# Performance work log

Hardware: AMD Instinct MI355X
Metric: run time of the kernel (lower is better)

The kernel has to match this reference:

```python
import jax, jax.numpy as jnp
import numpy as np


def log_mat_mul(m1, m2):
    """Log-semiring matmul: AND(a,b) = -logaddexp(-a,-b); OR-reduce = logsumexp over K.
    m1: (B, I, K), m2: (B, K, J) -> (B, I, J)."""
    # (B, I, 1, K) vs (B, 1, J, K)
    z = -jnp.logaddexp(-m1[:, :, None, :], -jnp.swapaxes(m2, -1, -2)[:, None, :, :])
    return jax.nn.logsumexp(z, axis=-1)


def cum_mul(m):
    """Parallel-doubling inclusive cumulative log-semiring product over axis 1.
    m: (B, L, D, D) -> (B, L, D, D) with m_out[:, j] = m[:,0] * ... * m[:,j]."""
    B, L, D, _ = m.shape
    step = 1
    while step < L:
        m4 = log_mat_mul(m[:, : L - step].reshape(-1, D, D),
                         m[:, step:].reshape(-1, D, D))
        m = jnp.concatenate([m[:, :step], m4.reshape(B, -1, D, D)], axis=1)
        step *= 2
    return m


def setup_inputs() -> dict:
    key = jax.random.key(0)
    k1, k2 = jax.random.split(key)
    B, L, D, A = 8, 64, 64, 4
    act = jax.random.randint(k1, (B, L), 0, A)  # action ids in [0, n_act)
    p = jax.random.normal(k2, (A + 1, D, D), dtype=jnp.float32)  # transition params
    init_vec = jnp.full((D,), 5.0, dtype=jnp.float32)            # nn.Parameter init
    return {"p": p, "init_vec": init_vec, "act": act}


def reference(p, init_vec, act):
    B, L = act.shape
    D = init_vec.shape[0]
    # state(act): gather per-step transition matrices (noise = 0.0)
    pm = p[act + 1]                      # (B, L, D, D)
    pm = cum_mul(pm)                     # cumulative products along L
    x = log_mat_mul(jnp.broadcast_to(init_vec.reshape(1, 1, D), (B * L, 1, D)),
                    pm.reshape(-1, D, D))  # (B*L, 1, D)
    x = x.reshape(B, L, D)
    # obs(state): one more log-semiring matmul against p[0]
    # y[b,l,j] = logsumexp_k( -logaddexp(-x[b,l,k], -p0[k,j]) )
    y = jax.nn.logsumexp(-jnp.logaddexp(-x[..., :, None], -p[0]), axis=-2)
    return y
```

## Files before the change

### kernel.cpp

```cpp
#include <hip/hip_runtime.h>
#include <hip/hip_bf16.h>


#define MAT 4096
#define NMAT 512
#define ARS 68
#define TBL_MATS 20

typedef float f32x2 __attribute__((ext_vector_type(2)));

__device__ __forceinline__ float rcpf(float x) { return __builtin_amdgcn_rcpf(x); }

__device__ __forceinline__ bool probe_f32(const void* initv) {
    return (*(const unsigned int*)initv) == 0x40A00000u;
}
__device__ __forceinline__ float load_in(const void* p, int i, bool isf32) {
    return isf32 ? ((const float*)p)[i]
                 : __bfloat162float(((const __hip_bfloat16*)p)[i]);
}

__device__ __forceinline__ const float* mat_src(int b, int x, int rnow,
                                                const float* bufA, const float* bufB,
                                                const float* tbl, const int* act) {
    const int la = (x == 0) ? 1 : (32 - __clz(x));
    const int lr = (la > rnow - 1) ? (rnow - 1) : la;
    if (lr == 1) {
        const float* T = tbl + b * TBL_MATS * MAT;
        if (x == 0) return T + act[b * 64] * MAT;
        return T + (4 + act[b * 64 + x - 1] * 4 + act[b * 64 + x]) * MAT;
    }
    const float* buf = (lr & 1) ? bufB : bufA;
    return buf + (b * 64 + x) * MAT;
}

__device__ __forceinline__ f32x2 quad2(const float a[4], f32x2 b0, f32x2 b1,
                                       f32x2 b2, f32x2 b3) {
#pragma clang fp contract(fast)
    const f32x2 x0 = b0 + a[0], x1 = b1 + a[1], x2 = b2 + a[2], x3 = b3 + a[3];
    const f32x2 n1 = x0 + x1, d1 = x0 * x1;
    const f32x2 n2 = x2 + x3, d2 = x2 * x3;
    const f32x2 num = n1 * d2 + n2 * d1;
    const f32x2 den = d1 * d2;
    f32x2 r;
    r.x = rcpf(den.x);
    r.y = rcpf(den.y);
    return num * r;
}

__device__ __forceinline__ void inner_round(const float* As, const float* Bs,
                                            int t, float4 out[2]) {
    const int r = t >> 4, c0 = (t & 15) * 4;
    f32x2 acc[2][2] = {{{0.f,0.f},{0.f,0.f}},{{0.f,0.f},{0.f,0.f}}};
    #pragma unroll
    for (int kq = 0; kq < 16; ++kq) {
        float a0[4], a1[4];
        f32x2 b[4][2];
        { const float4 v = *(const float4*)(As + r * ARS + kq * 4);
          a0[0]=v.x; a0[1]=v.y; a0[2]=v.z; a0[3]=v.w; }
        { const float4 v = *(const float4*)(As + (r + 16) * ARS + kq * 4);
          a1[0]=v.x; a1[1]=v.y; a1[2]=v.z; a1[3]=v.w; }
        #pragma unroll
        for (int kk = 0; kk < 4; ++kk) {
            const float4 v = *(const float4*)(Bs + (kq * 4 + kk) * 64 + c0);
            b[kk][0] = f32x2{v.x, v.y};
            b[kk][1] = f32x2{v.z, v.w};
        }
        #pragma unroll
        for (int cp = 0; cp < 2; ++cp) {
            acc[0][cp] += quad2(a0, b[0][cp], b[1][cp], b[2][cp], b[3][cp]);
            acc[1][cp] += quad2(a1, b[0][cp], b[1][cp], b[2][cp], b[3][cp]);
        }
    }
    out[0] = make_float4(rcpf(acc[0][0].x), rcpf(acc[0][0].y),
                         rcpf(acc[0][1].x), rcpf(acc[0][1].y));
    out[1] = make_float4(rcpf(acc[1][0].x), rcpf(acc[1][0].y),
                         rcpf(acc[1][1].x), rcpf(acc[1][1].y));
}

__device__ __forceinline__ void inner_full(const float* As, const float* Bs,
                                           int t, float4 out[4]) {
    const int r = t >> 4, c0 = (t & 15) * 4;
    f32x2 acc[4][2];
    #pragma unroll
    for (int i = 0; i < 4; ++i) { acc[i][0] = f32x2{0.f,0.f}; acc[i][1] = f32x2{0.f,0.f}; }
    #pragma unroll
    for (int kq = 0; kq < 16; ++kq) {
        float av[4][4];
        f32x2 b[4][2];
        #pragma unroll
        for (int i = 0; i < 4; ++i) {
            const float4 v = *(const float4*)(As + (r + i * 16) * ARS + kq * 4);
            av[i][0]=v.x; av[i][1]=v.y; av[i][2]=v.z; av[i][3]=v.w;
        }
        #pragma unroll
        for (int kk = 0; kk < 4; ++kk) {
            const float4 v = *(const float4*)(Bs + (kq * 4 + kk) * 64 + c0);
            b[kk][0] = f32x2{v.x, v.y};
            b[kk][1] = f32x2{v.z, v.w};
        }
        #pragma unroll
        for (int i = 0; i < 4; ++i)
            #pragma unroll
            for (int cp = 0; cp < 2; ++cp)
                acc[i][cp] += quad2(av[i], b[0][cp], b[1][cp], b[2][cp], b[3][cp]);
    }
    #pragma unroll
    for (int i = 0; i < 4; ++i)
        out[i] = make_float4(rcpf(acc[i][0].x), rcpf(acc[i][0].y),
                             rcpf(acc[i][1].x), rcpf(acc[i][1].y));
}

__device__ __forceinline__ void stage_A(float* As, const float* src, int t) {
    const float4* sa = (const float4*)src;
    #pragma unroll
    for (int i = 0; i < 2; ++i) {
        const int fi = t + i * 256;
        const float4 v = sa[fi];
        *(float4*)(As + (fi >> 4) * ARS + (fi & 15) * 4) = v;
    }
}
__device__ __forceinline__ void stage_B(float* Bs, const float* src, int t) {
    const float4* sb = (const float4*)src;
    #pragma unroll
    for (int i = 0; i < 4; ++i) ((float4*)Bs)[t + i * 256] = sb[t + i * 256];
}

__global__ __launch_bounds__(256, 4)
void k_table(const void* __restrict__ pIn, float* __restrict__ tbl,
             const void* __restrict__ initIn) {
    const bool isf32 = probe_f32(initIn);
    const int b = blockIdx.x & 7, job = blockIdx.x >> 3, t = threadIdx.x;
    float* T = tbl + b * TBL_MATS * MAT;

    if (job < 8) {
        const int a = job >> 1, rs = (job & 1) << 5;
        const int base = (a + 1) * MAT + rs * 64;
        float* d = T + a * MAT + rs * 64;
        #pragma unroll
        for (int i = 0; i < 8; ++i) {
            const int idx = t + i * 256;
            d[idx] = __expf(-load_in(pIn, base + idx, isf32));
        }
        return;
    }
    const int pj = job - 8, pairIdx = pj >> 1, rs = (pj & 1) << 5;
    const int a1 = pairIdx >> 2, a2 = pairIdx & 3;
    __shared__ float As[32 * ARS];
    __shared__ float Bs[MAT];
    const int baseA = (a1 + 1) * MAT + rs * 64;
    const int baseB = (a2 + 1) * MAT;
    #pragma unroll
    for (int i = 0; i < 8; ++i) {
        const int idx = t + i * 256;
        As[(idx >> 6) * ARS + (idx & 63)] = __expf(-load_in(pIn, baseA + idx, isf32));
    }
    #pragma unroll
    for (int i = 0; i < 16; ++i) {
        const int idx = t + i * 256;
        Bs[idx] = __expf(-load_in(pIn, baseB + idx, isf32));
    }
    __syncthreads();
    float4 o[2];
    inner_round(As, Bs, t, o);
    float* d = T + (4 + pairIdx) * MAT;
    const int r = t >> 4, c0 = (t & 15) * 4;
    *(float4*)(d + (rs + r) * 64 + c0) = o[0];
    *(float4*)(d + (rs + r + 16) * 64 + c0) = o[1];
}

__global__ __launch_bounds__(256, 4)
void k_round(const float* __restrict__ bufA, const float* __restrict__ bufB,
             const float* __restrict__ tbl, const int* __restrict__ act,
             float* __restrict__ dst, int step, int rnow) {
    const int t = threadIdx.x;
    const int b = blockIdx.x & 7, job = blockIdx.x >> 3;
    const int rs = (job & 1) << 5, mIdx = job >> 1;
    const int j = step + mIdx;
    const int m = b * 64 + j, ja = j - step;

    __shared__ float As[32 * ARS];
    __shared__ float Bs[MAT];
    stage_A(As, mat_src(b, ja, rnow, bufA, bufB, tbl, act) + rs * 64, t);
    stage_B(Bs, mat_src(b, j, rnow, bufA, bufB, tbl, act), t);
    __syncthreads();
    float4 o[2];
    inner_round(As, Bs, t, o);
    const int rr = t >> 4, c0 = (t & 15) * 4;
    *(float4*)(dst + m * MAT + (rs + rr) * 64 + c0) = o[0];
    *(float4*)(dst + m * MAT + (rs + rr + 16) * 64 + c0) = o[1];
}

__global__ __launch_bounds__(256, 2)
void k_final6(const float* __restrict__ bufA, const float* __restrict__ bufB,
              const float* __restrict__ tbl, const int* __restrict__ act,
              const void* __restrict__ pIn, const void* __restrict__ initIn,
              void* __restrict__ out) {
    const bool isf32 = probe_f32(initIn);
    const int t = threadIdx.x;
    const int b = blockIdx.x & 7, j = blockIdx.x >> 3;
    const int m = b * 64 + j;
    __shared__ float As[64 * ARS];
    __shared__ float Bs[MAT];
    __shared__ float red[4 * 64];
    __shared__ float uxs[64];
    __shared__ float uin[64];
    if (t < 64) uin[t] = __expf(-load_in(initIn, t, isf32));

    if (j >= 32) {
        const int ja = j - 32;
        const float* Asrc = mat_src(b, ja, 6, bufA, bufB, tbl, act);
        {
            const float4* sa = (const float4*)Asrc;
            #pragma unroll
            for (int i = 0; i < 4; ++i) {
                const int fi = t + i * 256;
                const float4 v = sa[fi];
                *(float4*)(As + (fi >> 4) * ARS + (fi & 15) * 4) = v;
            }
        }
        stage_B(Bs, mat_src(b, j, 6, bufA, bufB, tbl, act), t);
        __syncthreads();
        float4 o[4];
        inner_full(As, Bs, t, o);
        __syncthreads();
        const int r = t >> 4, c0 = (t & 15) * 4;
        #pragma unroll
        for (int i = 0; i < 4; ++i)
            *(float4*)(Bs + (r + i * 16) * 64 + c0) = o[i];
    } else {
        stage_B(Bs, mat_src(b, j, 7, bufA, bufB, tbl, act), t);
    }
    __syncthreads();

    const int jj = t & 63, kq = t >> 6;
    float s = 0.f;
    #pragma unroll
    for (int kk = 0; kk < 16; ++kk) {
        const int k = kq * 16 + kk;
        s += rcpf(uin[k] + Bs[k * 64 + jj]);
    }
    red[kq * 64 + jj] = s;
    __syncthreads();
    if (t < 64)
        uxs[t] = rcpf(((red[t] + red[64 + t]) + red[128 + t]) + red[192 + t]);
    __syncthreads();

    float s2 = 0.f;
    #pragma unroll
    for (int kk = 0; kk < 16; ++kk) {
        const int k = kq * 16 + kk;
        s2 += rcpf(uxs[k] + __expf(-load_in(pIn, k * 64 + jj, isf32)));
    }
    red[kq * 64 + jj] = s2;
    __syncthreads();
    if (t < 64) {
        const float y = __logf(((red[t] + red[64 + t]) + red[128 + t]) + red[192 + t]);
        if (isf32) ((float*)out)[m * 64 + t] = y;
        else       ((__hip_bfloat16*)out)[m * 64 + t] = __float2bfloat16(y);
    }
}

extern "C" void kernel_launch(void* const* d_in, const int* in_sizes, int n_in,
                              void* d_out, int out_size, void* d_ws, size_t ws_size,
                              hipStream_t stream) {
    const void* p = d_in[0];
    const void* initv = d_in[1];
    const int* act = (const int*)d_in[2];

    float* bufA = (float*)d_ws;
    float* bufB = bufA + NMAT * MAT;
    float* tbl  = bufB + NMAT * MAT;

    k_table<<<40 * 8, 256, 0, stream>>>(p, tbl, initv);
    k_round<<<62 * 2 * 8, 256, 0, stream>>>(bufA, bufB, tbl, act, bufA, 2, 2);
    k_round<<<60 * 2 * 8, 256, 0, stream>>>(bufA, bufB, tbl, act, bufB, 4, 3);
    k_round<<<56 * 2 * 8, 256, 0, stream>>>(bufA, bufB, tbl, act, bufA, 8, 4);
    k_round<<<48 * 2 * 8, 256, 0, stream>>>(bufA, bufB, tbl, act, bufB, 16, 5);
    k_final6<<<64 * 8, 256, 0, stream>>>(bufA, bufB, tbl, act, p, initv, d_out);
}
```

Baseline: 61.92 us.

## Fuse doubling scan rounds into three kernels with redundant in-block recomputation

Replaces the table kernel, four round kernels and final kernel with three 512-thread kernels. Each block recomputes up to two levels of the doubling scan locally in shared memory, so the three launches together cover the prefix products. This removes launch count and the global round-trips between rounds. In exchange, each block does up to three 64x64 semiring matmuls and needs more shared memory per block, which may lower occupancy.

```diff
diff --git a/kernel.cpp b/kernel.cpp
--- a/kernel.cpp
+++ b/kernel.cpp
@@ -5,7 +5,6 @@
 #define MAT 4096
 #define NMAT 512
 #define ARS 68
-#define TBL_MATS 20
 
 typedef float f32x2 __attribute__((ext_vector_type(2)));
 
@@ -17,20 +16,6 @@
 __device__ __forceinline__ float load_in(const void* p, int i, bool isf32) {
     return isf32 ? ((const float*)p)[i]
                  : __bfloat162float(((const __hip_bfloat16*)p)[i]);
-}
-
-__device__ __forceinline__ const float* mat_src(int b, int x, int rnow,
-                                                const float* bufA, const float* bufB,
-                                                const float* tbl, const int* act) {
-    const int la = (x == 0) ? 1 : (32 - __clz(x));
-    const int lr = (la > rnow - 1) ? (rnow - 1) : la;
-    if (lr == 1) {
-        const float* T = tbl + b * TBL_MATS * MAT;
-        if (x == 0) return T + act[b * 64] * MAT;
-        return T + (4 + act[b * 64 + x - 1] * 4 + act[b * 64 + x]) * MAT;
-    }
-    const float* buf = (lr & 1) ? bufB : bufA;
-    return buf + (b * 64 + x) * MAT;
 }
 
 __device__ __forceinline__ f32x2 quad2(const float a[4], f32x2 b0, f32x2 b1,
@@ -47,8 +32,8 @@
     return num * r;
 }
 
-__device__ __forceinline__ void inner_round(const float* As, const float* Bs,
-                                            int t, float4 out[2]) {
+__device__ __forceinline__ void inner512(const float* As, const float* Bs,
+                                         int t, float4 out[2]) {
     const int r = t >> 4, c0 = (t & 15) * 4;
     f32x2 acc[2][2] = {{{0.f,0.f},{0.f,0.f}},{{0.f,0.f},{0.f,0.f}}};
     #pragma unroll
@@ -57,7 +42,7 @@
         f32x2 b[4][2];
         { const float4 v = *(const float4*)(As + r * ARS + kq * 4);
           a0[0]=v.x; a0[1]=v.y; a0[2]=v.z; a0[3]=v.w; }
-        { const float4 v = *(const float4*)(As + (r + 16) * ARS + kq * 4);
+        { const float4 v = *(const float4*)(As + (r + 32) * ARS + kq * 4);
           a1[0]=v.x; a1[1]=v.y; a1[2]=v.z; a1[3]=v.w; }
         #pragma unroll
         for (int kk = 0; kk < 4; ++kk) {
@@ -77,184 +62,238 @@
                          rcpf(acc[1][1].x), rcpf(acc[1][1].y));
 }
 
-__device__ __forceinline__ void inner_full(const float* As, const float* Bs,
-                                           int t, float4 out[4]) {
+__device__ __forceinline__ void write2(float* dst, int stride, int t, const float4 o[2]) {
     const int r = t >> 4, c0 = (t & 15) * 4;
-    f32x2 acc[4][2];
-    #pragma unroll
-    for (int i = 0; i < 4; ++i) { acc[i][0] = f32x2{0.f,0.f}; acc[i][1] = f32x2{0.f,0.f}; }
-    #pragma unroll
-    for (int kq = 0; kq < 16; ++kq) {
-        float av[4][4];
-        f32x2 b[4][2];
-        #pragma unroll
-        for (int i = 0; i < 4; ++i) {
-            const float4 v = *(const float4*)(As + (r + i * 16) * ARS + kq * 4);
-            av[i][0]=v.x; av[i][1]=v.y; av[i][2]=v.z; av[i][3]=v.w;
-        }
-        #pragma unroll
-        for (int kk = 0; kk < 4; ++kk) {
-            const float4 v = *(const float4*)(Bs + (kq * 4 + kk) * 64 + c0);
-            b[kk][0] = f32x2{v.x, v.y};
-            b[kk][1] = f32x2{v.z, v.w};
-        }
-        #pragma unroll
-        for (int i = 0; i < 4; ++i)
-            #pragma unroll
-            for (int cp = 0; cp < 2; ++cp)
-                acc[i][cp] += quad2(av[i], b[0][cp], b[1][cp], b[2][cp], b[3][cp]);
-    }
-    #pragma unroll
-    for (int i = 0; i < 4; ++i)
-        out[i] = make_float4(rcpf(acc[i][0].x), rcpf(acc[i][0].y),
-                             rcpf(acc[i][1].x), rcpf(acc[i][1].y));
-}
-
-__device__ __forceinline__ void stage_A(float* As, const float* src, int t) {
-    const float4* sa = (const float4*)src;
+    *(float4*)(dst + r * stride + c0) = o[0];
+    *(float4*)(dst + (r + 32) * stride + c0) = o[1];
+}
+
+__device__ __forceinline__ void stage_pad(float* D, const float* src, int t) {
+    const float4* s = (const float4*)src;
     #pragma unroll
     for (int i = 0; i < 2; ++i) {
-        const int fi = t + i * 256;
-        const float4 v = sa[fi];
-        *(float4*)(As + (fi >> 4) * ARS + (fi & 15) * 4) = v;
-    }
-}
-__device__ __forceinline__ void stage_B(float* Bs, const float* src, int t) {
-    const float4* sb = (const float4*)src;
-    #pragma unroll
-    for (int i = 0; i < 4; ++i) ((float4*)Bs)[t + i * 256] = sb[t + i * 256];
-}
-
-__global__ __launch_bounds__(256, 4)
-void k_table(const void* __restrict__ pIn, float* __restrict__ tbl,
-             const void* __restrict__ initIn) {
+        const int fi = t + i * 512;
+        const float4 v = s[fi];
+        *(float4*)(D + (fi >> 4) * ARS + (fi & 15) * 4) = v;
+    }
+}
+__device__ __forceinline__ void stage_row(float* D, const float* src, int t) {
+    const float4* s = (const float4*)src;
+    ((float4*)D)[t] = s[t];
+    ((float4*)D)[t + 512] = s[t + 512];
+}
+__device__ __forceinline__ void stage_pad_exp(float* D, const void* p, int base,
+                                              bool isf32, int t) {
+    #pragma unroll
+    for (int i = 0; i < 8; ++i) {
+        const int idx = t + i * 512;
+        D[(idx >> 6) * ARS + (idx & 63)] = __expf(-load_in(p, base + idx, isf32));
+    }
+}
+__device__ __forceinline__ void stage_row_exp(float* D, const void* p, int base,
+                                              bool isf32, int t) {
+    #pragma unroll
+    for (int i = 0; i < 8; ++i) {
+        const int idx = t + i * 512;
+        D[idx] = __expf(-load_in(p, base + idx, isf32));
+    }
+}
+
+__global__ __launch_bounds__(512, 4)
+void k1(const void* __restrict__ pIn, const int* __restrict__ act,
+        float* __restrict__ bufA, float* __restrict__ bufB,
+        const void* __restrict__ initIn) {
     const bool isf32 = probe_f32(initIn);
-    const int b = blockIdx.x & 7, job = blockIdx.x >> 3, t = threadIdx.x;
-    float* T = tbl + b * TBL_MATS * MAT;
-
-    if (job < 8) {
-        const int a = job >> 1, rs = (job & 1) << 5;
-        const int base = (a + 1) * MAT + rs * 64;
-        float* d = T + a * MAT + rs * 64;
+    const int t = threadIdx.x, b = blockIdx.x & 7, j = blockIdx.x >> 3;
+    const int m = b * 64 + j;
+    const int* a = act + b * 64;
+    __shared__ float As[64 * ARS];
+    __shared__ float Ds[64 * ARS];
+    __shared__ float Bs[MAT];
+    __shared__ float Es[MAT];
+
+    if (j == 0) {
+        const int base = (a[0] + 1) * MAT;
+        float* d = bufB + m * MAT;
         #pragma unroll
         for (int i = 0; i < 8; ++i) {
-            const int idx = t + i * 256;
+            const int idx = t + i * 512;
             d[idx] = __expf(-load_in(pIn, base + idx, isf32));
         }
         return;
     }
-    const int pj = job - 8, pairIdx = pj >> 1, rs = (pj & 1) << 5;
-    const int a1 = pairIdx >> 2, a2 = pairIdx & 3;
-    __shared__ float As[32 * ARS];
-    __shared__ float Bs[MAT];
-    const int baseA = (a1 + 1) * MAT + rs * 64;
-    const int baseB = (a2 + 1) * MAT;
-    #pragma unroll
-    for (int i = 0; i < 8; ++i) {
-        const int idx = t + i * 256;
-        As[(idx >> 6) * ARS + (idx & 63)] = __expf(-load_in(pIn, baseA + idx, isf32));
-    }
-    #pragma unroll
-    for (int i = 0; i < 16; ++i) {
-        const int idx = t + i * 256;
-        Bs[idx] = __expf(-load_in(pIn, baseB + idx, isf32));
+    if (j == 1) {
+        stage_pad_exp(As, pIn, (a[0] + 1) * MAT, isf32, t);
+        stage_row_exp(Bs, pIn, (a[1] + 1) * MAT, isf32, t);
+        __syncthreads();
+        float4 o[2];
+        inner512(As, Bs, t, o);
+        write2(bufB + m * MAT, 64, t, o);
+        return;
+    }
+    if (j == 2) {
+        stage_pad_exp(Ds, pIn, (a[0] + 1) * MAT, isf32, t);
+    } else {
+        stage_pad_exp(As, pIn, (a[j - 3] + 1) * MAT, isf32, t);
+        stage_row_exp(Bs, pIn, (a[j - 2] + 1) * MAT, isf32, t);
+        __syncthreads();
+        float4 o[2];
+        inner512(As, Bs, t, o);
+        write2(Ds, ARS, t, o);
+    }
+    __syncthreads();
+    stage_pad_exp(As, pIn, (a[j - 1] + 1) * MAT, isf32, t);
+    stage_row_exp(Bs, pIn, (a[j] + 1) * MAT, isf32, t);
+    __syncthreads();
+    {
+        float4 o[2];
+        inner512(As, Bs, t, o);
+        write2(Es, 64, t, o);
     }
     __syncthreads();
     float4 o[2];
-    inner_round(As, Bs, t, o);
-    float* d = T + (4 + pairIdx) * MAT;
-    const int r = t >> 4, c0 = (t & 15) * 4;
-    *(float4*)(d + (rs + r) * 64 + c0) = o[0];
-    *(float4*)(d + (rs + r + 16) * 64 + c0) = o[1];
-}
-
-__global__ __launch_bounds__(256, 4)
-void k_round(const float* __restrict__ bufA, const float* __restrict__ bufB,
-             const float* __restrict__ tbl, const int* __restrict__ act,
-             float* __restrict__ dst, int step, int rnow) {
-    const int t = threadIdx.x;
-    const int b = blockIdx.x & 7, job = blockIdx.x >> 3;
-    const int rs = (job & 1) << 5, mIdx = job >> 1;
-    const int j = step + mIdx;
-    const int m = b * 64 + j, ja = j - step;
-
-    __shared__ float As[32 * ARS];
-    __shared__ float Bs[MAT];
-    stage_A(As, mat_src(b, ja, rnow, bufA, bufB, tbl, act) + rs * 64, t);
-    stage_B(Bs, mat_src(b, j, rnow, bufA, bufB, tbl, act), t);
-    __syncthreads();
-    float4 o[2];
-    inner_round(As, Bs, t, o);
-    const int rr = t >> 4, c0 = (t & 15) * 4;
-    *(float4*)(dst + m * MAT + (rs + rr) * 64 + c0) = o[0];
-    *(float4*)(dst + m * MAT + (rs + rr + 16) * 64 + c0) = o[1];
-}
-
-__global__ __launch_bounds__(256, 2)
-void k_final6(const float* __restrict__ bufA, const float* __restrict__ bufB,
-              const float* __restrict__ tbl, const int* __restrict__ act,
-              const void* __restrict__ pIn, const void* __restrict__ initIn,
-              void* __restrict__ out) {
-    const bool isf32 = probe_f32(initIn);
-    const int t = threadIdx.x;
-    const int b = blockIdx.x & 7, j = blockIdx.x >> 3;
+    inner512(Ds, Es, t, o);
+    write2(bufA + m * MAT, 64, t, o);
+}
+
+__global__ __launch_bounds__(512, 4)
+void k2(const float* __restrict__ bufA, float* __restrict__ bufB) {
+    const int t = threadIdx.x, b = blockIdx.x & 7, j = (blockIdx.x >> 3) + 4;
     const int m = b * 64 + j;
     __shared__ float As[64 * ARS];
+    __shared__ float Ds[64 * ARS];
     __shared__ float Bs[MAT];
-    __shared__ float red[4 * 64];
+    __shared__ float Es[MAT];
+
+    #define R2P(y) (((y) < 2 ? bufB : bufA) + (b * 64 + (y)) * MAT)
+
+    if (j < 8) {
+        stage_pad(As, R2P(j - 4), t);
+        stage_row(Bs, R2P(j), t);
+        __syncthreads();
+        float4 o[2];
+        inner512(As, Bs, t, o);
+        write2(bufB + m * MAT, 64, t, o);
+        return;
+    }
+    const int ja = j - 8;
+    if (ja < 4) {
+        stage_pad(Ds, R2P(ja), t);
+    } else {
+        stage_pad(As, R2P(ja - 4), t);
+        stage_row(Bs, R2P(ja), t);
+        __syncthreads();
+        float4 o[2];
+        inner512(As, Bs, t, o);
+        write2(Ds, ARS, t, o);
+    }
+    __syncthreads();
+    stage_pad(As, R2P(j - 4), t);
+    stage_row(Bs, R2P(j), t);
+    __syncthreads();
+    {
+        float4 o[2];
+        inner512(As, Bs, t, o);
+        write2(Es, 64, t, o);
+    }
+    __syncthreads();
+    float4 o[2];
+    inner512(Ds, Es, t, o);
+    write2(bufB + m * MAT, 64, t, o);
+    #undef R2P
+}
+
+__global__ __launch_bounds__(512, 4)
+void k3(const float* __restrict__ bufA, const float* __restrict__ bufB,
+        const void* __restrict__ pIn, const void* __restrict__ initIn,
+        void* __restrict__ out) {
+    const bool isf32 = probe_f32(initIn);
+    const int t = threadIdx.x, b = blockIdx.x & 7, j = blockIdx.x >> 3;
+    const int m = b * 64 + j;
+    __shared__ float As[64 * ARS];
+    __shared__ float Ds[64 * ARS];
+    __shared__ float Bs[MAT];
+    __shared__ float Es[MAT];
+    __shared__ float red[8 * 64];
     __shared__ float uxs[64];
     __shared__ float uin[64];
     if (t < 64) uin[t] = __expf(-load_in(initIn, t, isf32));
 
-    if (j >= 32) {
+    #define ST4(x) ((((x) == 2) || ((x) == 3) ? bufA : bufB) + (b * 64 + (x)) * MAT)
+
+    const float* Up;
+    if (j < 16) {
+        stage_row(Es, ST4(j), t);
+        Up = Es;
+        __syncthreads();
+    } else if (j < 32) {
+        stage_pad(As, ST4(j - 16), t);
+        stage_row(Bs, ST4(j), t);
+        __syncthreads();
+        float4 o[2];
+        inner512(As, Bs, t, o);
+        write2(Es, 64, t, o);
+        Up = Es;
+        __syncthreads();
+    } else {
         const int ja = j - 32;
-        const float* Asrc = mat_src(b, ja, 6, bufA, bufB, tbl, act);
+        if (ja < 16) {
+            stage_pad(Ds, ST4(ja), t);
+        } else {
+            stage_pad(As, ST4(ja - 16), t);
+            stage_row(Bs, ST4(ja), t);
+            __syncthreads();
+            float4 o[2];
+            inner512(As, Bs, t, o);
+            write2(Ds, ARS, t, o);
+            __syncthreads();
+        }
+        stage_pad(As, ST4(j - 16), t);
+        stage_row(Bs, ST4(j), t);
+        __syncthreads();
         {
-            const float4* sa = (const float4*)Asrc;
-            #pragma unroll
-            for (int i = 0; i < 4; ++i) {
-                const int fi = t + i * 256;
-                const float4 v = sa[fi];
-                *(float4*)(As + (fi >> 4) * ARS + (fi & 15) * 4) = v;
-            }
-        }
-        stage_B(Bs, mat_src(b, j, 6, bufA, bufB, tbl, act), t);
-        __syncthreads();
-        float4 o[4];
-        inner_full(As, Bs, t, o);
-        __syncthreads();
-        const int r = t >> 4, c0 = (t & 15) * 4;
-        #pragma unroll
-        for (int i = 0; i < 4; ++i)
-            *(float4*)(Bs + (r + i * 16) * 64 + c0) = o[i];
-    } else {
-        stage_B(Bs, mat_src(b, j, 7, bufA, bufB, tbl, act), t);
-    }
-    __syncthreads();
+            float4 o[2];
+            inner512(As, Bs, t, o);
+            write2(Es, 64, t, o);
+        }
+        __syncthreads();
+        float4 o[2];
+        inner512(Ds, Es, t, o);
+        write2(As, 64, t, o);
+        Up = As;
+        __syncthreads();
+    }
+    #undef ST4
 
     const int jj = t & 63, kq = t >> 6;
     float s = 0.f;
     #pragma unroll
-    for (int kk = 0; kk < 16; ++kk) {
-        const int k = kq * 16 + kk;
-        s += rcpf(uin[k] + Bs[k * 64 + jj]);
+    for (int kk = 0; kk < 8; ++kk) {
+        const int k = kq * 8 + kk;
+        s += rcpf(uin[k] + Up[k * 64 + jj]);
     }
     red[kq * 64 + jj] = s;
     __syncthreads();
-    if (t < 64)
-        uxs[t] = rcpf(((red[t] + red[64 + t]) + red[128 + t]) + red[192 + t]);
-    __syncthreads();
-
+    if (t < 64) {
+        float acc = red[t];
+        #pragma unroll
+        for (int q = 1; q < 8; ++q) acc += red[q * 64 + t];
+        uxs[t] = rcpf(acc);
+    }
+    __syncthreads();
     float s2 = 0.f;
     #pragma unroll
-    for (int kk = 0; kk < 16; ++kk) {
-        const int k = kq * 16 + kk;
+    for (int kk = 0; kk < 8; ++kk) {
+        const int k = kq * 8 + kk;
         s2 += rcpf(uxs[k] + __expf(-load_in(pIn, k * 64 + jj, isf32)));
     }
     red[kq * 64 + jj] = s2;
     __syncthreads();
     if (t < 64) {
-        const float y = __logf(((red[t] + red[64 + t]) + red[128 + t]) + red[192 + t]);
+        float acc = red[t];
+        #pragma unroll
+        for (int q = 1; q < 8; ++q) acc += red[q * 64 + t];
+        const float y = __logf(acc);
         if (isf32) ((float*)out)[m * 64 + t] = y;
         else       ((__hip_bfloat16*)out)[m * 64 + t] = __float2bfloat16(y);
     }
@@ -269,12 +308,8 @@
 
     float* bufA = (float*)d_ws;
     float* bufB = bufA + NMAT * MAT;
-    float* tbl  = bufB + NMAT * MAT;
-
-    k_table<<<40 * 8, 256, 0, stream>>>(p, tbl, initv);
-    k_round<<<62 * 2 * 8, 256, 0, stream>>>(bufA, bufB, tbl, act, bufA, 2, 2);
-    k_round<<<60 * 2 * 8, 256, 0, stream>>>(bufA, bufB, tbl, act, bufB, 4, 3);
-    k_round<<<56 * 2 * 8, 256, 0, stream>>>(bufA, bufB, tbl, act, bufA, 8, 4);
-    k_round<<<48 * 2 * 8, 256, 0, stream>>>(bufA, bufB, tbl, act, bufB, 16, 5);
-    k_final6<<<64 * 8, 256, 0, stream>>>(bufA, bufB, tbl, act, p, initv, d_out);
-}
+
+    k1<<<8 * 64, 512, 0, stream>>>(p, act, bufA, bufB, initv);
+    k2<<<8 * 60, 512, 0, stream>>>(bufA, bufB);
+    k3<<<8 * 64, 512, 0, stream>>>(bufA, bufB, p, initv, d_out);
+}
```

Result: slower. 84.83 us (+37.0%).

## Fuse last doubling round into final kernel, recomputing step-16 products per block

Applied to the files above, without the earlier changes.

Removes the step-16 round launch and folds its work into the final kernel. Each block recomputes the round-5 products it needs from round-4 data, for up to three full 64x64 log-semiring matmuls per block in the upper half. This saves one kernel launch and a global write/read of the intermediate buffer. In exchange it adds redundant compute, uneven per-block work, and more shared memory, which may reduce occupancy.

```diff
diff --git a/kernel.cpp b/kernel.cpp
--- a/kernel.cpp
+++ b/kernel.cpp
@@ -110,10 +110,26 @@
                              rcpf(acc[i][1].x), rcpf(acc[i][1].y));
 }
 
+__device__ __forceinline__ void write4(float* dst, int stride, int t, const float4 o[4]) {
+    const int r = t >> 4, c0 = (t & 15) * 4;
+    #pragma unroll
+    for (int i = 0; i < 4; ++i)
+        *(float4*)(dst + (r + i * 16) * stride + c0) = o[i];
+}
+
 __device__ __forceinline__ void stage_A(float* As, const float* src, int t) {
     const float4* sa = (const float4*)src;
     #pragma unroll
     for (int i = 0; i < 2; ++i) {
+        const int fi = t + i * 256;
+        const float4 v = sa[fi];
+        *(float4*)(As + (fi >> 4) * ARS + (fi & 15) * 4) = v;
+    }
+}
+__device__ __forceinline__ void stage_Afull(float* As, const float* src, int t) {
+    const float4* sa = (const float4*)src;
+    #pragma unroll
+    for (int i = 0; i < 4; ++i) {
         const int fi = t + i * 256;
         const float4 v = sa[fi];
         *(float4*)(As + (fi >> 4) * ARS + (fi & 15) * 4) = v;
@@ -191,53 +207,76 @@
 }
 
 __global__ __launch_bounds__(256, 2)
-void k_final6(const float* __restrict__ bufA, const float* __restrict__ bufB,
-              const float* __restrict__ tbl, const int* __restrict__ act,
-              const void* __restrict__ pIn, const void* __restrict__ initIn,
-              void* __restrict__ out) {
+void k_final56(const float* __restrict__ bufA, const float* __restrict__ bufB,
+               const float* __restrict__ tbl, const int* __restrict__ act,
+               const void* __restrict__ pIn, const void* __restrict__ initIn,
+               void* __restrict__ out) {
     const bool isf32 = probe_f32(initIn);
     const int t = threadIdx.x;
     const int b = blockIdx.x & 7, j = blockIdx.x >> 3;
     const int m = b * 64 + j;
     __shared__ float As[64 * ARS];
+    __shared__ float Ds[64 * ARS];
     __shared__ float Bs[MAT];
+    __shared__ float Es[MAT];
     __shared__ float red[4 * 64];
     __shared__ float uxs[64];
     __shared__ float uin[64];
     if (t < 64) uin[t] = __expf(-load_in(initIn, t, isf32));
 
-    if (j >= 32) {
-        const int ja = j - 32;
-        const float* Asrc = mat_src(b, ja, 6, bufA, bufB, tbl, act);
-        {
-            const float4* sa = (const float4*)Asrc;
-            #pragma unroll
-            for (int i = 0; i < 4; ++i) {
-                const int fi = t + i * 256;
-                const float4 v = sa[fi];
-                *(float4*)(As + (fi >> 4) * ARS + (fi & 15) * 4) = v;
-            }
-        }
-        stage_B(Bs, mat_src(b, j, 6, bufA, bufB, tbl, act), t);
+    #define ST(x) mat_src(b, (x), 5, bufA, bufB, tbl, act)
+
+    const float* Up;
+    if (j < 16) {
+        stage_B(Es, ST(j), t);
+        Up = Es;
+        __syncthreads();
+    } else if (j < 32) {
+        stage_Afull(As, ST(j - 16), t);
+        stage_B(Bs, ST(j), t);
         __syncthreads();
         float4 o[4];
         inner_full(As, Bs, t, o);
-        __syncthreads();
-        const int r = t >> 4, c0 = (t & 15) * 4;
-        #pragma unroll
-        for (int i = 0; i < 4; ++i)
-            *(float4*)(Bs + (r + i * 16) * 64 + c0) = o[i];
+        write4(Es, 64, t, o);
+        Up = Es;
+        __syncthreads();
     } else {
-        stage_B(Bs, mat_src(b, j, 7, bufA, bufB, tbl, act), t);
-    }
-    __syncthreads();
+        const int ja = j - 32;
+        if (ja < 16) {
+            stage_Afull(Ds, ST(ja), t);
+            __syncthreads();
+        } else {
+            stage_Afull(As, ST(ja - 16), t);
+            stage_B(Bs, ST(ja), t);
+            __syncthreads();
+            float4 o[4];
+            inner_full(As, Bs, t, o);
+            write4(Ds, ARS, t, o);
+            __syncthreads();
+        }
+        stage_Afull(As, ST(j - 16), t);
+        stage_B(Bs, ST(j), t);
+        __syncthreads();
+        {
+            float4 o[4];
+            inner_full(As, Bs, t, o);
+            write4(Es, 64, t, o);
+        }
+        __syncthreads();
+        float4 o[4];
+        inner_full(Ds, Es, t, o);
+        write4(Bs, 64, t, o);
+        Up = Bs;
+        __syncthreads();
+    }
+    #undef ST
 
     const int jj = t & 63, kq = t >> 6;
     float s = 0.f;
     #pragma unroll
     for (int kk = 0; kk < 16; ++kk) {
         const int k = kq * 16 + kk;
-        s += rcpf(uin[k] + Bs[k * 64 + jj]);
+        s += rcpf(uin[k] + Up[k * 64 + jj]);
     }
     red[kq * 64 + jj] = s;
     __syncthreads();
@@ -275,6 +314,5 @@
     k_round<<<62 * 2 * 8, 256, 0, stream>>>(bufA, bufB, tbl, act, bufA, 2, 2);
     k_round<<<60 * 2 * 8, 256, 0, stream>>>(bufA, bufB, tbl, act, bufB, 4, 3);
     k_round<<<56 * 2 * 8, 256, 0, stream>>>(bufA, bufB, tbl, act, bufA, 8, 4);
-    k_round<<<48 * 2 * 8, 256, 0, stream>>>(bufA, bufB, tbl, act, bufB, 16, 5);
-    k_final6<<<64 * 8, 256, 0, stream>>>(bufA, bufB, tbl, act, p, initv, d_out);
-}
+    k_final56<<<64 * 8, 256, 0, stream>>>(bufA, bufB, tbl, act, p, initv, d_out);
+}
```

Result: slower. 67.88 us (+9.6%).
